# Kernel tuning notes

Hardware: AMD Instinct MI355X
Metric: run time of the kernel (lower is better)

## Reference

```python
import jax, jax.numpy as jnp
import numpy as np

N_NODES = 100000
HIDDEN = 128


def gcn_conv(x, edge_index, W, b, n_nodes):
    """PyG GCNConv: out = D^{-1/2} (A+I) D^{-1/2} (x @ W) + b."""
    src, dst = edge_index[0], edge_index[1]
    # add self-loops
    loop = jnp.arange(n_nodes, dtype=src.dtype)
    src = jnp.concatenate([src, loop])
    dst = jnp.concatenate([dst, loop])
    # degree of (A + I) w.r.t. destination nodes
    deg = jax.ops.segment_sum(jnp.ones_like(dst, dtype=x.dtype), dst,
                              num_segments=n_nodes)
    dinv = jax.lax.rsqrt(jnp.where(deg > 0, deg, 1.0))
    norm = dinv[src] * dinv[dst]  # [E+N]
    h = x @ W                      # [N, F_out]
    msg = h[src] * norm[:, None]   # gather + scale, [E+N, F_out]
    out = jax.ops.segment_sum(msg, dst, num_segments=n_nodes)
    return out + b


def setup_inputs() -> dict:
    key = jax.random.key(0)
    k1, k2, k3, k4, k5, k6 = jax.random.split(key, 6)
    num_features, num_classes = 128, 40
    n_edges = 1600000
    x = jax.random.normal(k1, (N_NODES, num_features), dtype=jnp.float32)
    edge_index = jax.random.randint(k2, (2, n_edges), 0, N_NODES, dtype=jnp.int64)
    s1 = 1.0 / np.sqrt(num_features)
    s2 = 1.0 / np.sqrt(HIDDEN)
    W1 = jax.random.uniform(k3, (num_features, HIDDEN), jnp.float32, -s1, s1)
    b1 = jax.random.uniform(k4, (HIDDEN,), jnp.float32, -s1, s1)
    W2 = jax.random.uniform(k5, (HIDDEN, num_classes), jnp.float32, -s2, s2)
    b2 = jax.random.uniform(k6, (num_classes,), jnp.float32, -s2, s2)
    return {"x": x, "edge_index": edge_index, "W1": W1, "b1": b1,
            "W2": W2, "b2": b2}


def reference(x, edge_index, W1, b1, W2, b2):
    n = x.shape[0]
    h = gcn_conv(x, edge_index, W1, b1, n)
    h = jax.nn.relu(h)
    # dropout is identity in eval mode (training=False)
    out = gcn_conv(h, edge_index, W2, b2, n)
    return out
```

## Files before the change

kernel.cpp:

```cpp
#include <hip/hip_runtime.h>

typedef short s16x8 __attribute__((ext_vector_type(8)));
typedef float f32x4 __attribute__((ext_vector_type(4)));
typedef float f32x2 __attribute__((ext_vector_type(2)));


__device__ inline unsigned pack_bf16(float a, float b) {
  unsigned ua = __float_as_uint(a), ub = __float_as_uint(b);
  ua += 0x7fffu + ((ua >> 16) & 1u);
  ub += 0x7fffu + ((ub >> 16) & 1u);
  return (ua >> 16) | (ub & 0xffff0000u);
}
__device__ inline float unpack_lo(unsigned u) { return __uint_as_float(u << 16); }
__device__ inline float unpack_hi(unsigned u) { return __uint_as_float(u & 0xffff0000u); }


__global__ void kb_count(const int* __restrict__ dst, int E,
                         int* __restrict__ bucket_cnt, int NB) {
  __shared__ int h[256];
  h[threadIdx.x] = 0;
  __syncthreads();
  int i = blockIdx.x * blockDim.x + threadIdx.x;
  int stride = gridDim.x * blockDim.x;
  for (; i < E; i += stride) atomicAdd(&h[dst[i] >> 9], 1);
  __syncthreads();
  if (threadIdx.x < NB && h[threadIdx.x]) atomicAdd(&bucket_cnt[threadIdx.x], h[threadIdx.x]);
}

__global__ void kb_scan(const int* __restrict__ bucket_cnt, int NB, int E,
                        int* __restrict__ bucket_start, int* __restrict__ bucket_cursor) {
  int tid = threadIdx.x, lane = tid & 63, w = tid >> 6;
  int v = (tid < NB) ? bucket_cnt[tid] : 0;
  int x = v;
#pragma unroll
  for (int off = 1; off < 64; off <<= 1) {
    int u = __shfl_up(x, off);
    if (lane >= off) x += u;
  }
  __shared__ int ws4[4];
  if (lane == 63) ws4[w] = x;
  __syncthreads();
  int add = 0;
  for (int k = 0; k < w; ++k) add += ws4[k];
  x += add;
  int excl = x - v;
  if (tid < NB) {
    bucket_start[tid] = excl;
    bucket_cursor[tid] = excl;
  }
  if (tid == 0) bucket_start[NB] = E;
}

__global__ __launch_bounds__(256) void kb_scatter(const int* __restrict__ src,
                                                  const int* __restrict__ dst, int E,
                                                  int* __restrict__ bucket_cursor,
                                                  unsigned* __restrict__ pairs) {
  constexpr int T = 16;
  __shared__ int bin_cnt[256], bin_base[256];
  bin_cnt[threadIdx.x] = 0;
  __syncthreads();
  int base = blockIdx.x * (256 * T);
  unsigned u[T];
  int bb[T], slot[T];
#pragma unroll
  for (int t = 0; t < T; ++t) {
    int e = base + t * 256 + threadIdx.x;
    if (e < E) {
      int s = src[e], d = dst[e];
      bb[t] = d >> 9;
      u[t] = (unsigned)s | ((unsigned)(d & 511) << 17);
      slot[t] = atomicAdd(&bin_cnt[bb[t]], 1);
    } else {
      bb[t] = -1;
    }
  }
  __syncthreads();
  if (bin_cnt[threadIdx.x] > 0)
    bin_base[threadIdx.x] = atomicAdd(&bucket_cursor[threadIdx.x], bin_cnt[threadIdx.x]);
  __syncthreads();
#pragma unroll
  for (int t = 0; t < T; ++t)
    if (bb[t] >= 0) pairs[bin_base[bb[t]] + slot[t]] = u[t];
}

__global__ __launch_bounds__(256) void kc_csr(const unsigned* __restrict__ pairs,
                                              const int* __restrict__ bucket_start,
                                              int N, float* __restrict__ dinv,
                                              int* __restrict__ row_start,
                                              int* __restrict__ deg,
                                              int* __restrict__ col) {
  int b = blockIdx.x;
  int pbase = bucket_start[b], m = bucket_start[b + 1] - pbase;
  int tid = threadIdx.x, lane = tid & 63, w = tid >> 6;
  __shared__ int cnt[512], cur[512];
  __shared__ int ws4[4];
  cnt[tid] = 0;
  cnt[tid + 256] = 0;
  __syncthreads();
  for (int i = tid; i < m; i += 256) atomicAdd(&cnt[pairs[pbase + i] >> 17], 1);
  __syncthreads();
  int c0 = cnt[2 * tid], c1 = cnt[2 * tid + 1];
  int p = c0 + c1, x = p;
#pragma unroll
  for (int off = 1; off < 64; off <<= 1) {
    int uu = __shfl_up(x, off);
    if (lane >= off) x += uu;
  }
  if (lane == 63) ws4[w] = x;
  __syncthreads();
  int add = 0;
  for (int k = 0; k < w; ++k) add += ws4[k];
  x += add;
  int xe = x - p;
  cur[2 * tid] = xe;
  cur[2 * tid + 1] = xe + c0;
  int n0 = b * 512 + 2 * tid;
  if (n0 < N) {
    deg[n0] = c0;
    dinv[n0] = rsqrtf((float)(c0 + 1));
    row_start[n0] = pbase + xe;
  }
  if (n0 + 1 < N) {
    deg[n0 + 1] = c1;
    dinv[n0 + 1] = rsqrtf((float)(c1 + 1));
    row_start[n0 + 1] = pbase + xe + c0;
  }
  __syncthreads();
  for (int i = tid; i < m; i += 256) {
    unsigned uu = pairs[pbase + i];
    int pos = atomicAdd(&cur[uu >> 17], 1);
    col[pbase + pos] = (int)(uu & 131071u);
  }
}


__global__ void kw_trans(const float* __restrict__ W, int NC, int NT,
                         unsigned* __restrict__ WT) {
  int id = blockIdx.x * 256 + threadIdx.x;
  if (id >= NT * 64) return;
  int n = id >> 6, kd = id & 63;
  float a = 0.f, b = 0.f;
  if (n < NC) {
    a = W[(2 * kd) * NC + n];
    b = W[(2 * kd + 1) * NC + n];
  }
  WT[id] = pack_bf16(a, b);
}


template <int NTILES, int GSTRIDE, int NCOLS, bool A_FP32>
__global__ __launch_bounds__(256, 4) void k_gemm_mfma(const void* __restrict__ Ain,
                                                      const unsigned* __restrict__ WT,
                                                      const float* __restrict__ dinv,
                                                      unsigned* __restrict__ G, int N) {
  __shared__ unsigned Ws[NTILES * 16 * 68];
  __shared__ unsigned As[64 * 68];

  const int tid = threadIdx.x;
  const int row0 = blockIdx.x * 64;

  constexpr int WV2 = NTILES * 16 * 32;
  const uint2* WT2 = (const uint2*)WT;
#pragma unroll
  for (int i = tid; i < WV2; i += 256) {
    int r = i >> 5, kd2 = i & 31;
    *(uint2*)&Ws[r * 68 + kd2 * 2] = WT2[i];
  }

  if (A_FP32) {
    const float4* X4 = (const float4*)Ain + (size_t)row0 * 32;
#pragma unroll
    for (int i = tid; i < 2048; i += 256) {
      int r = i >> 5, c4 = i & 31;
      uint2 o = {0u, 0u};
      if (row0 + r < N) {
        float4 xv = X4[i];
        o.x = pack_bf16(xv.x, xv.y);
        o.y = pack_bf16(xv.z, xv.w);
      }
      *(uint2*)&As[r * 68 + c4 * 2] = o;
    }
  } else {
    const uint2* H2 = (const uint2*)Ain + (size_t)row0 * 32;
#pragma unroll
    for (int i = tid; i < 2048; i += 256) {
      int r = i >> 5, kd2 = i & 31;
      uint2 o = {0u, 0u};
      if (row0 + r < N) o = H2[i];
      *(uint2*)&As[r * 68 + kd2 * 2] = o;
    }
  }
  __syncthreads();

  const int w = tid >> 6, lane = tid & 63;
  const int quad = lane >> 4, n16 = lane & 15;

  f32x4 acc[NTILES];
#pragma unroll
  for (int t = 0; t < NTILES; ++t) acc[t] = {0.f, 0.f, 0.f, 0.f};

  const char* Ab = (const char*)As + (w * 16 + n16) * 272 + quad * 16;
  const char* Bb = (const char*)Ws + n16 * 272 + quad * 16;
#pragma unroll
  for (int s = 0; s < 4; ++s) {
    s16x8 a = *(const s16x8*)(Ab + s * 64);
#pragma unroll
    for (int t = 0; t < NTILES; ++t) {
      s16x8 b = *(const s16x8*)(Bb + t * 16 * 272 + s * 64);
      acc[t] = __builtin_amdgcn_mfma_f32_16x16x32_bf16(a, b, acc[t], 0, 0, 0);
    }
  }

#pragma unroll
  for (int reg = 0; reg < 4; ++reg) {
    int r = row0 + w * 16 + quad * 4 + reg;
    float dv = (r < N) ? dinv[r] : 0.f;
#pragma unroll
    for (int t = 0; t < NTILES; ++t) {
      float v = acc[t][reg] * dv;
      float vp = __shfl_xor(v, 1);
      int colc = t * 16 + n16;
      if ((n16 & 1) == 0 && colc < NCOLS && r < N)
        G[(size_t)r * GSTRIDE + t * 8 + (n16 >> 1)] = pack_bf16(v, vp);
    }
  }
}


__global__ __launch_bounds__(256) void k_agg1(const unsigned* __restrict__ g1,
                                              const int* __restrict__ row_start,
                                              const int* __restrict__ deg,
                                              const int* __restrict__ col,
                                              const float* __restrict__ dinv,
                                              const float* __restrict__ b1,
                                              unsigned* __restrict__ h2, int N) {
  int node = blockIdx.x * 4 + (threadIdx.x >> 6);
  if (node >= N) return;
  const int lane = threadIdx.x & 63;
  const int g = lane >> 4;
  const unsigned boff = (unsigned)(lane & 15) * 16u;
  const char* __restrict__ g1b = (const char*)g1;

  f32x2 acc0 = {0.f, 0.f}, acc1 = {0.f, 0.f}, acc2 = {0.f, 0.f}, acc3 = {0.f, 0.f};

#define ACC4(U)                                          \
  acc0 += (f32x2){unpack_lo((U).x), unpack_hi((U).x)};   \
  acc1 += (f32x2){unpack_lo((U).y), unpack_hi((U).y)};   \
  acc2 += (f32x2){unpack_lo((U).z), unpack_hi((U).z)};   \
  acc3 += (f32x2){unpack_lo((U).w), unpack_hi((U).w)};

  if (g == 0) {
    uint4 su = *(const uint4*)(g1b + ((((unsigned)node) << 8) | boff));
    ACC4(su);
  }

  const int start = row_start[node], cnt = deg[node];
  if (cnt > 0) {
    const int last = start + cnt - 1;
    int j = 0;
    for (;;) {
      int ci = start + j + lane;
      int cv = col[ci < last ? ci : last];
      int rem = cnt - j;
      if (rem >= 64) {
#pragma unroll
        for (int s = 0; s < 16; s += 4) {
          int c0 = __shfl(cv, s * 4 + g);
          int c1 = __shfl(cv, s * 4 + 4 + g);
          int c2 = __shfl(cv, s * 4 + 8 + g);
          int c3 = __shfl(cv, s * 4 + 12 + g);
          uint4 u0 = *(const uint4*)(g1b + ((((unsigned)c0) << 8) | boff));
          uint4 u1 = *(const uint4*)(g1b + ((((unsigned)c1) << 8) | boff));
          uint4 u2 = *(const uint4*)(g1b + ((((unsigned)c2) << 8) | boff));
          uint4 u3 = *(const uint4*)(g1b + ((((unsigned)c3) << 8) | boff));
          ACC4(u0);
          ACC4(u1);
          ACC4(u2);
          ACC4(u3);
        }
        j += 64;
        if (j >= cnt) break;
        continue;
      }
      int fs = rem >> 2;
      int s = 0;
      for (; s + 4 <= fs; s += 4) {
        int c0 = __shfl(cv, s * 4 + g);
        int c1 = __shfl(cv, s * 4 + 4 + g);
        int c2 = __shfl(cv, s * 4 + 8 + g);
        int c3 = __shfl(cv, s * 4 + 12 + g);
        uint4 u0 = *(const uint4*)(g1b + ((((unsigned)c0) << 8) | boff));
        uint4 u1 = *(const uint4*)(g1b + ((((unsigned)c1) << 8) | boff));
        uint4 u2 = *(const uint4*)(g1b + ((((unsigned)c2) << 8) | boff));
        uint4 u3 = *(const uint4*)(g1b + ((((unsigned)c3) << 8) | boff));
        ACC4(u0);
        ACC4(u1);
        ACC4(u2);
        ACC4(u3);
      }
      if (s + 2 <= fs) {
        int c0 = __shfl(cv, s * 4 + g);
        int c1 = __shfl(cv, s * 4 + 4 + g);
        uint4 u0 = *(const uint4*)(g1b + ((((unsigned)c0) << 8) | boff));
        uint4 u1 = *(const uint4*)(g1b + ((((unsigned)c1) << 8) | boff));
        ACC4(u0);
        ACC4(u1);
        s += 2;
      }
      if (s < fs) {
        int c0 = __shfl(cv, s * 4 + g);
        uint4 u0 = *(const uint4*)(g1b + ((((unsigned)c0) << 8) | boff));
        ACC4(u0);
        ++s;
      }
      int pr = rem & 3;
      int cpr = __shfl(cv, fs * 4 + g);
      if (g < pr) {
        uint4 u0 = *(const uint4*)(g1b + ((((unsigned)cpr) << 8) | boff));
        ACC4(u0);
      }
      break;
    }
  }
#undef ACC4

  acc0.x += __shfl_xor(acc0.x, 16);
  acc0.y += __shfl_xor(acc0.y, 16);
  acc1.x += __shfl_xor(acc1.x, 16);
  acc1.y += __shfl_xor(acc1.y, 16);
  acc2.x += __shfl_xor(acc2.x, 16);
  acc2.y += __shfl_xor(acc2.y, 16);
  acc3.x += __shfl_xor(acc3.x, 16);
  acc3.y += __shfl_xor(acc3.y, 16);
  acc0.x += __shfl_xor(acc0.x, 32);
  acc0.y += __shfl_xor(acc0.y, 32);
  acc1.x += __shfl_xor(acc1.x, 32);
  acc1.y += __shfl_xor(acc1.y, 32);
  acc2.x += __shfl_xor(acc2.x, 32);
  acc2.y += __shfl_xor(acc2.y, 32);
  acc3.x += __shfl_xor(acc3.x, 32);
  acc3.y += __shfl_xor(acc3.y, 32);

  if (g == 0) {
    float dn = dinv[node];
    int r4 = (lane & 15) * 4;
    const float2* bp = (const float2*)b1;
    float2 bb0 = bp[r4 + 0];
    float2 bb1 = bp[r4 + 1];
    float2 bb2 = bp[r4 + 2];
    float2 bb3 = bp[r4 + 3];
    uint4 o;
    o.x = pack_bf16(fmaxf(fmaf(acc0.x, dn, bb0.x), 0.f), fmaxf(fmaf(acc0.y, dn, bb0.y), 0.f));
    o.y = pack_bf16(fmaxf(fmaf(acc1.x, dn, bb1.x), 0.f), fmaxf(fmaf(acc1.y, dn, bb1.y), 0.f));
    o.z = pack_bf16(fmaxf(fmaf(acc2.x, dn, bb2.x), 0.f), fmaxf(fmaf(acc2.y, dn, bb2.y), 0.f));
    o.w = pack_bf16(fmaxf(fmaf(acc3.x, dn, bb3.x), 0.f), fmaxf(fmaf(acc3.y, dn, bb3.y), 0.f));
    *(uint4*)(h2 + (size_t)node * 64 + r4) = o;
  }
}


__global__ __launch_bounds__(256) void k_agg2(const unsigned* __restrict__ g2,
                                              const int* __restrict__ row_start,
                                              const int* __restrict__ deg,
                                              const int* __restrict__ col,
                                              const float* __restrict__ dinv,
                                              const float* __restrict__ b2,
                                              float* __restrict__ out, int N) {
  const int lane = threadIdx.x & 63;
  const int wv = threadIdx.x >> 6;
  const int g = lane / 5;
  const int r = lane - g * 5;
  const int node = (blockIdx.x * 4 + wv) * 12 + g;
  if (g >= 12 || node >= N) return;
  const unsigned rb = (unsigned)r * 16u;
  const char* __restrict__ gb = (const char*)g2;

  f32x2 a0 = {0.f, 0.f}, a1 = {0.f, 0.f}, a2 = {0.f, 0.f}, a3 = {0.f, 0.f};

#define ACC4(U)                                         \
  a0 += (f32x2){unpack_lo((U).x), unpack_hi((U).x)};    \
  a1 += (f32x2){unpack_lo((U).y), unpack_hi((U).y)};    \
  a2 += (f32x2){unpack_lo((U).z), unpack_hi((U).z)};    \
  a3 += (f32x2){unpack_lo((U).w), unpack_hi((U).w)};

  {
    uint4 su = *(const uint4*)(gb + (unsigned)node * 80u + rb);
    ACC4(su);
  }

  const int start = row_start[node], cnt = deg[node];
  const int* __restrict__ cp = col + start;
  int j = 0;
  for (; j + 8 <= cnt; j += 8) {
    int c0 = cp[j], c1 = cp[j + 1], c2 = cp[j + 2], c3 = cp[j + 3];
    int c4 = cp[j + 4], c5 = cp[j + 5], c6 = cp[j + 6], c7 = cp[j + 7];
    uint4 u0 = *(const uint4*)(gb + (unsigned)c0 * 80u + rb);
    uint4 u1 = *(const uint4*)(gb + (unsigned)c1 * 80u + rb);
    uint4 u2 = *(const uint4*)(gb + (unsigned)c2 * 80u + rb);
    uint4 u3 = *(const uint4*)(gb + (unsigned)c3 * 80u + rb);
    uint4 u4 = *(const uint4*)(gb + (unsigned)c4 * 80u + rb);
    uint4 u5 = *(const uint4*)(gb + (unsigned)c5 * 80u + rb);
    uint4 u6 = *(const uint4*)(gb + (unsigned)c6 * 80u + rb);
    uint4 u7 = *(const uint4*)(gb + (unsigned)c7 * 80u + rb);
    ACC4(u0);
    ACC4(u1);
    ACC4(u2);
    ACC4(u3);
    ACC4(u4);
    ACC4(u5);
    ACC4(u6);
    ACC4(u7);
  }
  if (j + 4 <= cnt) {
    int c0 = cp[j], c1 = cp[j + 1], c2 = cp[j + 2], c3 = cp[j + 3];
    uint4 u0 = *(const uint4*)(gb + (unsigned)c0 * 80u + rb);
    uint4 u1 = *(const uint4*)(gb + (unsigned)c1 * 80u + rb);
    uint4 u2 = *(const uint4*)(gb + (unsigned)c2 * 80u + rb);
    uint4 u3 = *(const uint4*)(gb + (unsigned)c3 * 80u + rb);
    ACC4(u0);
    ACC4(u1);
    ACC4(u2);
    ACC4(u3);
    j += 4;
  }
  for (; j < cnt; ++j) {
    int c = cp[j];
    uint4 u = *(const uint4*)(gb + (unsigned)c * 80u + rb);
    ACC4(u);
  }
#undef ACC4

  const float dn = dinv[node];
  const float4* __restrict__ bp = (const float4*)(b2 + 8 * r);
  float4 bq0 = bp[0], bq1 = bp[1];
  float4 o0, o1;
  o0.x = fmaf(a0.x, dn, bq0.x);
  o0.y = fmaf(a0.y, dn, bq0.y);
  o0.z = fmaf(a1.x, dn, bq0.z);
  o0.w = fmaf(a1.y, dn, bq0.w);
  o1.x = fmaf(a2.x, dn, bq1.x);
  o1.y = fmaf(a2.y, dn, bq1.y);
  o1.z = fmaf(a3.x, dn, bq1.z);
  o1.w = fmaf(a3.y, dn, bq1.w);
  float* op = out + (size_t)node * 40 + 8 * r;
  *(float4*)op = o0;
  *(float4*)(op + 4) = o1;
}


extern "C" void kernel_launch(void* const* d_in, const int* in_sizes, int n_in,
                              void* d_out, int out_size, void* d_ws, size_t ws_size,
                              hipStream_t stream) {
  const float* x = (const float*)d_in[0];
  const int* ei = (const int*)d_in[1];
  const float* W1 = (const float*)d_in[2];
  const float* b1 = (const float*)d_in[3];
  const float* W2 = (const float*)d_in[4];
  const float* b2 = (const float*)d_in[5];

  const int F = in_sizes[3];
  const int N = in_sizes[0] / F;
  const int E = in_sizes[1] / 2;
  const int* esrc = ei;
  const int* edst = ei + E;
  const int NB = (N + 511) / 512;

  char* ws = (char*)d_ws;
  int* bucket_cnt = (int*)(ws + 0);
  int* bucket_start = (int*)(ws + 4096);
  int* bucket_cursor = (int*)(ws + 8192);
  unsigned* w1t = (unsigned*)(ws + 16384);
  unsigned* w2t = (unsigned*)(ws + 49152);
  float* dinv = (float*)(ws + 65536);
  int* row_start = (int*)(ws + 466944);
  int* deg = (int*)(ws + 868352);
  unsigned* pairs = (unsigned*)(ws + 1269760);
  int* colx = (int*)(ws + 7669760);
  unsigned* g1 = (unsigned*)(ws + 14073856);
  unsigned* h2 = (unsigned*)(ws + 39673856);
  unsigned* g2 = g1;

  (void)hipMemsetAsync(bucket_cnt, 0, 1024, stream);

  kb_count<<<256, 256, 0, stream>>>(edst, E, bucket_cnt, NB);
  kb_scan<<<1, 256, 0, stream>>>(bucket_cnt, NB, E, bucket_start, bucket_cursor);
  kb_scatter<<<(E + 4095) / 4096, 256, 0, stream>>>(esrc, edst, E, bucket_cursor, pairs);
  kc_csr<<<NB, 256, 0, stream>>>(pairs, bucket_start, N, dinv, row_start, deg, colx);

  kw_trans<<<32, 256, 0, stream>>>(W1, 128, 128, w1t);
  kw_trans<<<12, 256, 0, stream>>>(W2, 40, 48, w2t);

  const int gblocks = (N + 63) / 64;
  k_gemm_mfma<8, 64, 128, true><<<gblocks, 256, 0, stream>>>(x, w1t, dinv, g1, N);
  k_agg1<<<(N + 3) / 4, 256, 0, stream>>>(g1, row_start, deg, colx, dinv, b1, h2, N);
  k_gemm_mfma<3, 20, 40, false><<<gblocks, 256, 0, stream>>>(h2, w2t, dinv, g2, N);
  k_agg2<<<(N + 47) / 48, 256, 0, stream>>>(g2, row_start, deg, colx, dinv, b2,
                                            (float*)d_out, N);
}
```

Baseline: 298.2 us.

## Halve CSR bucket width and read GEMM weights directly from global memory

The CSR build now uses 256-node buckets instead of 512, which doubles the bucket count to about 391 and doubles the block count for kc_csr. The count, scan and scatter kernels are widened to match, with 512-entry shared histograms and a 512-thread scan. The GEMM kernel no longer stages transposed weights in LDS; MFMA B operands are loaded straight from global/L2, which saves LDS and a staging pass but adds repeated global reads per wave. Workspace offsets are unchanged, and bucket_start now holds up to 392 entries, which still fits in its 4 KB slot.

```diff
diff --git a/kernel.cpp b/kernel.cpp
--- a/kernel.cpp
+++ b/kernel.cpp
@@ -17,14 +17,17 @@
 
 __global__ void kb_count(const int* __restrict__ dst, int E,
                          int* __restrict__ bucket_cnt, int NB) {
-  __shared__ int h[256];
+  __shared__ int h[512];
   h[threadIdx.x] = 0;
+  h[threadIdx.x + 256] = 0;
   __syncthreads();
   int i = blockIdx.x * blockDim.x + threadIdx.x;
   int stride = gridDim.x * blockDim.x;
-  for (; i < E; i += stride) atomicAdd(&h[dst[i] >> 9], 1);
-  __syncthreads();
-  if (threadIdx.x < NB && h[threadIdx.x]) atomicAdd(&bucket_cnt[threadIdx.x], h[threadIdx.x]);
+  for (; i < E; i += stride) atomicAdd(&h[dst[i] >> 8], 1);
+  __syncthreads();
+  int i0 = threadIdx.x, i1 = threadIdx.x + 256;
+  if (i0 < NB && h[i0]) atomicAdd(&bucket_cnt[i0], h[i0]);
+  if (i1 < NB && h[i1]) atomicAdd(&bucket_cnt[i1], h[i1]);
 }
 
 __global__ void kb_scan(const int* __restrict__ bucket_cnt, int NB, int E,
@@ -37,11 +40,11 @@
     int u = __shfl_up(x, off);
     if (lane >= off) x += u;
   }
-  __shared__ int ws4[4];
-  if (lane == 63) ws4[w] = x;
+  __shared__ int ws8[8];
+  if (lane == 63) ws8[w] = x;
   __syncthreads();
   int add = 0;
-  for (int k = 0; k < w; ++k) add += ws4[k];
+  for (int k = 0; k < w; ++k) add += ws8[k];
   x += add;
   int excl = x - v;
   if (tid < NB) {
@@ -56,8 +59,9 @@
                                                   int* __restrict__ bucket_cursor,
                                                   unsigned* __restrict__ pairs) {
   constexpr int T = 16;
-  __shared__ int bin_cnt[256], bin_base[256];
+  __shared__ int bin_cnt[512], bin_base[512];
   bin_cnt[threadIdx.x] = 0;
+  bin_cnt[threadIdx.x + 256] = 0;
   __syncthreads();
   int base = blockIdx.x * (256 * T);
   unsigned u[T];
@@ -67,16 +71,17 @@
     int e = base + t * 256 + threadIdx.x;
     if (e < E) {
       int s = src[e], d = dst[e];
-      bb[t] = d >> 9;
-      u[t] = (unsigned)s | ((unsigned)(d & 511) << 17);
+      bb[t] = d >> 8;
+      u[t] = (unsigned)s | ((unsigned)(d & 255) << 17);
       slot[t] = atomicAdd(&bin_cnt[bb[t]], 1);
     } else {
       bb[t] = -1;
     }
   }
   __syncthreads();
-  if (bin_cnt[threadIdx.x] > 0)
-    bin_base[threadIdx.x] = atomicAdd(&bucket_cursor[threadIdx.x], bin_cnt[threadIdx.x]);
+  int i0 = threadIdx.x, i1 = threadIdx.x + 256;
+  if (bin_cnt[i0] > 0) bin_base[i0] = atomicAdd(&bucket_cursor[i0], bin_cnt[i0]);
+  if (bin_cnt[i1] > 0) bin_base[i1] = atomicAdd(&bucket_cursor[i1], bin_cnt[i1]);
   __syncthreads();
 #pragma unroll
   for (int t = 0; t < T; ++t)
@@ -92,15 +97,14 @@
   int b = blockIdx.x;
   int pbase = bucket_start[b], m = bucket_start[b + 1] - pbase;
   int tid = threadIdx.x, lane = tid & 63, w = tid >> 6;
-  __shared__ int cnt[512], cur[512];
+  __shared__ int cnt[256], cur[256];
   __shared__ int ws4[4];
   cnt[tid] = 0;
-  cnt[tid + 256] = 0;
   __syncthreads();
   for (int i = tid; i < m; i += 256) atomicAdd(&cnt[pairs[pbase + i] >> 17], 1);
   __syncthreads();
-  int c0 = cnt[2 * tid], c1 = cnt[2 * tid + 1];
-  int p = c0 + c1, x = p;
+  int v = cnt[tid];
+  int x = v;
 #pragma unroll
   for (int off = 1; off < 64; off <<= 1) {
     int uu = __shfl_up(x, off);
@@ -111,19 +115,13 @@
   int add = 0;
   for (int k = 0; k < w; ++k) add += ws4[k];
   x += add;
-  int xe = x - p;
-  cur[2 * tid] = xe;
-  cur[2 * tid + 1] = xe + c0;
-  int n0 = b * 512 + 2 * tid;
+  int excl = x - v;
+  cur[tid] = excl;
+  int n0 = b * 256 + tid;
   if (n0 < N) {
-    deg[n0] = c0;
-    dinv[n0] = rsqrtf((float)(c0 + 1));
-    row_start[n0] = pbase + xe;
-  }
-  if (n0 + 1 < N) {
-    deg[n0 + 1] = c1;
-    dinv[n0 + 1] = rsqrtf((float)(c1 + 1));
-    row_start[n0 + 1] = pbase + xe + c0;
+    deg[n0] = v;
+    dinv[n0] = rsqrtf((float)(v + 1));
+    row_start[n0] = pbase + excl;
   }
   __syncthreads();
   for (int i = tid; i < m; i += 256) {
@@ -153,19 +151,10 @@
                                                       const unsigned* __restrict__ WT,
                                                       const float* __restrict__ dinv,
                                                       unsigned* __restrict__ G, int N) {
-  __shared__ unsigned Ws[NTILES * 16 * 68];
   __shared__ unsigned As[64 * 68];
 
   const int tid = threadIdx.x;
   const int row0 = blockIdx.x * 64;
-
-  constexpr int WV2 = NTILES * 16 * 32;
-  const uint2* WT2 = (const uint2*)WT;
-#pragma unroll
-  for (int i = tid; i < WV2; i += 256) {
-    int r = i >> 5, kd2 = i & 31;
-    *(uint2*)&Ws[r * 68 + kd2 * 2] = WT2[i];
-  }
 
   if (A_FP32) {
     const float4* X4 = (const float4*)Ain + (size_t)row0 * 32;
@@ -200,13 +189,13 @@
   for (int t = 0; t < NTILES; ++t) acc[t] = {0.f, 0.f, 0.f, 0.f};
 
   const char* Ab = (const char*)As + (w * 16 + n16) * 272 + quad * 16;
-  const char* Bb = (const char*)Ws + n16 * 272 + quad * 16;
+  const char* Bg = (const char*)WT + n16 * 256 + quad * 16;
 #pragma unroll
   for (int s = 0; s < 4; ++s) {
     s16x8 a = *(const s16x8*)(Ab + s * 64);
 #pragma unroll
     for (int t = 0; t < NTILES; ++t) {
-      s16x8 b = *(const s16x8*)(Bb + t * 16 * 272 + s * 64);
+      s16x8 b = *(const s16x8*)(Bg + t * 4096 + s * 64);
       acc[t] = __builtin_amdgcn_mfma_f32_16x16x32_bf16(a, b, acc[t], 0, 0, 0);
     }
   }
@@ -463,7 +452,7 @@
   const int E = in_sizes[1] / 2;
   const int* esrc = ei;
   const int* edst = ei + E;
-  const int NB = (N + 511) / 512;
+  const int NB = (N + 255) / 256;
 
   char* ws = (char*)d_ws;
   int* bucket_cnt = (int*)(ws + 0);
@@ -480,10 +469,10 @@
   unsigned* h2 = (unsigned*)(ws + 39673856);
   unsigned* g2 = g1;
 
-  (void)hipMemsetAsync(bucket_cnt, 0, 1024, stream);
+  (void)hipMemsetAsync(bucket_cnt, 0, 2048, stream);
 
   kb_count<<<256, 256, 0, stream>>>(edst, E, bucket_cnt, NB);
-  kb_scan<<<1, 256, 0, stream>>>(bucket_cnt, NB, E, bucket_start, bucket_cursor);
+  kb_scan<<<1, 512, 0, stream>>>(bucket_cnt, NB, E, bucket_start, bucket_cursor);
   kb_scatter<<<(E + 4095) / 4096, 256, 0, stream>>>(esrc, edst, E, bucket_cursor, pairs);
   kc_csr<<<NB, 256, 0, stream>>>(pairs, bucket_start, N, dinv, row_start, deg, colx);
 
```

Measured after the change: 303.3 us. Within noise of the previous version (+1.7%).
